# Performance work log

Measured on AMD Instinct MI355X. Metric: run time of the kernel, lower is better.

The kernel has to match this reference:

```python
import jax, jax.numpy as jnp
import numpy as np

PAD = 1  # deform_conv2d called with stride=1, padding=1, dilation=1 in forward


def _bilinear_gather(x, py, px):
    """Bilinear sample x [B,C,H,W] at float coords py,px [B,K,Ho,Wo].
    Out-of-bounds corners contribute zero (torchvision deform_conv2d semantics).
    Returns [B,C,K,Ho,Wo]."""
    B, C, H, W = x.shape
    y0 = jnp.floor(py)
    x0 = jnp.floor(px)
    y1, x1 = y0 + 1.0, x0 + 1.0
    wy1 = py - y0
    wy0 = 1.0 - wy1
    wx1 = px - x0
    wx0 = 1.0 - wx1
    x_flat = x.reshape(B, C, H * W)

    def corner(yi, xi, w):
        m = ((yi >= 0) & (yi < H) & (xi >= 0) & (xi < W)).astype(x.dtype)
        yc = jnp.clip(yi, 0, H - 1).astype(jnp.int32)
        xc = jnp.clip(xi, 0, W - 1).astype(jnp.int32)
        lin = (yc * W + xc).reshape(B, -1)  # [B, K*Ho*Wo]
        vals = jax.vmap(lambda xf, idx: jnp.take(xf, idx, axis=1))(x_flat, lin)
        vals = vals.reshape(B, C, *yi.shape[1:])  # [B,C,K,Ho,Wo]
        return vals * (w * m)[:, None]

    return (corner(y0, x0, wy0 * wx0) + corner(y0, x1, wy0 * wx1)
            + corner(y1, x0, wy1 * wx0) + corner(y1, x1, wy1 * wx1))


def reference(x, w_off, b_off, weight):
    B, C, H, W = x.shape
    O, Ci, kh, kw = weight.shape
    K = kh * kw
    # offset conv: Conv2d(C -> 2*k*k, kernel 3, stride 1, pad 1, groups=1)
    offset = jax.lax.conv_general_dilated(
        x, w_off, window_strides=(1, 1), padding=[(PAD, PAD), (PAD, PAD)],
        dimension_numbers=('NCHW', 'OIHW', 'NCHW')) + b_off[None, :, None, None]
    off = offset.reshape(B, K, 2, H, W)  # channel layout: (tap, [dy, dx])

    ky = jnp.repeat(jnp.arange(kh, dtype=x.dtype), kw)  # [K] kernel row index
    kx = jnp.tile(jnp.arange(kw, dtype=x.dtype), kh)    # [K] kernel col index
    ys = jnp.arange(H, dtype=x.dtype)[None, None, :, None]  # [1,1,H,1]
    xs = jnp.arange(W, dtype=x.dtype)[None, None, None, :]  # [1,1,1,W]
    py = ys + (ky - PAD)[None, :, None, None] + off[:, :, 0]  # [B,K,H,W]
    px = xs + (kx - PAD)[None, :, None, None] + off[:, :, 1]

    sampled = _bilinear_gather(x, py, px)  # [B,C,K,H,W]
    out = jnp.einsum('bckhw,ock->bohw', sampled, weight.reshape(O, Ci, K))
    return out


def setup_inputs() -> dict:
    key = jax.random.key(0)
    k1, k2, k3 = jax.random.split(key, 3)
    x = jax.random.normal(k1, (4, 64, 128, 128), dtype=jnp.float32)
    # small offset-conv weights -> modest learned offsets (realistic DCN behavior)
    w_off = jax.random.normal(k2, (18, 64, 3, 3), dtype=jnp.float32) * 0.01
    b_off = jnp.zeros((18,), dtype=jnp.float32)
    weight = jax.random.normal(k3, (64, 64, 3, 3), dtype=jnp.float32)
    return {'x': x, 'w_off': w_off, 'b_off': b_off, 'weight': weight}
```

## Files before the change

### kernel.cpp

```cpp
#include <hip/hip_runtime.h>
#include <math.h>

typedef _Float16 f16;
typedef _Float16 f16x8 __attribute__((ext_vector_type(8)));
typedef float f32x4 __attribute__((ext_vector_type(4)));

namespace {
constexpr int Bn = 4;
constexpr int Cn = 64;
constexpr int On = 64;
constexpr int Hn = 128;
constexpr int Wn = 128;
constexpr int Kn = 9;
constexpr int HWn = Hn * Wn;
constexpr int CKn = Cn * Kn;
constexpr int NPIX = Bn * HWn;
constexpr int SR = 72;
}

__global__ __launch_bounds__(256) void prep_weights(
    const float* __restrict__ w_off, const float* __restrict__ weight,
    f16* __restrict__ wofb, f16* __restrict__ wtb) {
  int t = blockIdx.x * 256 + threadIdx.x;
  if (t < Kn * On * Cn) {
    int c = t & 63, o = (t >> 6) & 63, k = t >> 12;
    wtb[t] = (f16)weight[((o << 6) + c) * 9 + k];
  }
  if (t < Kn * 32 * Cn) {
    int c = t & 63, o = (t >> 6) & 31, k = t >> 11;
    float v = (o < 18) ? w_off[((o << 6) + c) * 9 + k] : 0.f;
    wofb[t] = (f16)v;
  }
}

__global__ __launch_bounds__(256) void transpose_x(
    const float* __restrict__ x, f16* __restrict__ xt) {
  const int l = threadIdx.x & 63;
  const int cw = threadIdx.x >> 6;
  const int pixbase = blockIdx.x * 64;
  const int b = pixbase >> 14;
  const int hw = (pixbase & (HWn - 1)) + l;

  f16x8 v0, v1;
#pragma unroll
  for (int i = 0; i < 8; ++i) {
    v0[i] = (f16)x[((size_t)(b * Cn + cw * 16 + i)) * HWn + hw];
    v1[i] = (f16)x[((size_t)(b * Cn + cw * 16 + 8 + i)) * HWn + hw];
  }
  f16* dst = xt + ((size_t)(b * HWn + hw)) * 64 + cw * 16;
  *(f16x8*)dst = v0;
  *(f16x8*)(dst + 8) = v1;
}

__global__ __launch_bounds__(256) void offset_mfma(
    const f16* __restrict__ xt, const f16* __restrict__ wofb,
    const float* __restrict__ b_off, float* __restrict__ offset) {
  __shared__ __align__(16) f16 Sb[2][64 * SR];
  __shared__ __align__(16) f16 Wb[2][32 * SR];

  const int t = threadIdx.x;
  const int pixbase = blockIdx.x * 64;
  const int b = pixbase >> 14;
  const int y = (pixbase & (HWn - 1)) >> 7;
  const int xx0 = pixbase & (Wn - 1);
  const f16* xb = xt + ((size_t)b * HWn) * 64;

  const int px_s = t >> 2, cq = t & 3;
  const int lane = t & 63, wv = t >> 6;
  const int l15 = lane & 15, q = lane >> 4;
  const int m = wv & 1;
  const int nb = (wv >> 1) * 2;

  auto stage = [&](int k, int buf) {
    const int dy = k / 3 - 1, dx = k % 3 - 1;
    const int ys = y + dy, xs = xx0 + px_s + dx;
    f16* sdst = &Sb[buf][px_s * SR + cq * 16];
    if (ys >= 0 && ys < Hn && xs >= 0 && xs < Wn) {
      const f16* src = xb + (size_t)(ys * Wn + xs) * 64 + cq * 16;
      *(f16x8*)sdst = *(const f16x8*)src;
      *(f16x8*)(sdst + 8) = *(const f16x8*)(src + 8);
    } else {
      f16x8 z = {};
      *(f16x8*)sdst = z;
      *(f16x8*)(sdst + 8) = z;
    }
    const int o = t >> 3, part = t & 7;
    const f16* wsrc = wofb + (((size_t)(k * 32 + o)) << 6) + part * 8;
    *(f16x8*)&Wb[buf][o * SR + part * 8] = *(const f16x8*)wsrc;
  };

  f32x4 acc[2];
#pragma unroll
  for (int t2 = 0; t2 < 2; ++t2) acc[t2] = (f32x4){0.f, 0.f, 0.f, 0.f};

  stage(0, 0);
  __syncthreads();
  for (int k = 0; k < Kn; ++k) {
    const int cur = k & 1;
    if (k + 1 < Kn) stage(k + 1, 1 - cur);
#pragma unroll
    for (int s = 0; s < 2; ++s) {
      f16x8 af = *(const f16x8*)&Wb[cur][(m * 16 + l15) * SR + s * 32 + q * 8];
#pragma unroll
      for (int t2 = 0; t2 < 2; ++t2) {
        f16x8 bf = *(const f16x8*)
            &Sb[cur][((nb + t2) * 16 + l15) * SR + s * 32 + q * 8];
        acc[t2] = __builtin_amdgcn_mfma_f32_16x16x32_f16(af, bf, acc[t2],
                                                         0, 0, 0);
      }
    }
    __syncthreads();
  }

  float* ob = offset + ((size_t)b * HWn + y * Wn + xx0) * 18;
#pragma unroll
  for (int t2 = 0; t2 < 2; ++t2) {
#pragma unroll
    for (int r = 0; r < 4; ++r) {
      int o = m * 16 + q * 4 + r;
      if (o < 18) {
        int pxl = (nb + t2) * 16 + l15;
        ob[(size_t)pxl * 18 + o] = acc[t2][r] + b_off[o];
      }
    }
  }
}

__global__ __launch_bounds__(256, 4) void dcn_main(
    const f16* __restrict__ xt, const float* __restrict__ offset,
    const f16* __restrict__ wtb, float* __restrict__ out) {
  __shared__ __align__(16) f16 Sb[2][64 * SR];
  __shared__ __align__(16) f16 Wb[2][64 * SR];

  const int t = threadIdx.x;
  const int px_s = t >> 2, cq = t & 3;
  const int pxg = blockIdx.x * 64 + px_s;
  const int b = pxg >> 14;
  const int rem = pxg & (HWn - 1);
  const int y = rem >> 7;
  const int xx = rem & (Wn - 1);
  const f16* xb = xt + (((size_t)b) << 14) * 64;

  const int lane = t & 63, wv = t >> 6;
  const int l15 = lane & 15, q = lane >> 4;
  const int obase = wv * 16;

  float2 off9[9];
  {
    const float* ofp = offset + (size_t)pxg * 18;
#pragma unroll
    for (int k = 0; k < Kn; ++k) off9[k] = *(const float2*)(ofp + 2 * k);
  }

  auto stage = [&](int k, int buf) {
    const int dy = k / 3 - 1, dx = k % 3 - 1;
    float py = (float)(y + dy) + off9[k].x;
    float pxf = (float)(xx + dx) + off9[k].y;
    float y0f = floorf(py), x0f = floorf(pxf);
    int y0 = (int)y0f, x0 = (int)x0f;
    int y1 = y0 + 1, x1 = x0 + 1;
    float wy1 = py - y0f, wx1 = pxf - x0f;
    float wy0 = 1.f - wy1, wx0 = 1.f - wx1;
    float my0 = (y0 >= 0 && y0 < Hn) ? 1.f : 0.f;
    float my1 = (y1 >= 0 && y1 < Hn) ? 1.f : 0.f;
    float mx0 = (x0 >= 0 && x0 < Wn) ? 1.f : 0.f;
    float mx1 = (x1 >= 0 && x1 < Wn) ? 1.f : 0.f;
    float w00 = wy0 * wx0 * my0 * mx0;
    float w01 = wy0 * wx1 * my0 * mx1;
    float w10 = wy1 * wx0 * my1 * mx0;
    float w11 = wy1 * wx1 * my1 * mx1;
    int cy0 = min(max(y0, 0), Hn - 1), cy1 = min(max(y1, 0), Hn - 1);
    int cx0 = min(max(x0, 0), Wn - 1), cx1 = min(max(x1, 0), Wn - 1);
    const f16* r00 = xb + (size_t)(cy0 * Wn + cx0) * 64 + cq * 16;
    const f16* r01 = xb + (size_t)(cy0 * Wn + cx1) * 64 + cq * 16;
    const f16* r10 = xb + (size_t)(cy1 * Wn + cx0) * 64 + cq * 16;
    const f16* r11 = xb + (size_t)(cy1 * Wn + cx1) * 64 + cq * 16;
    f16* sdst = &Sb[buf][px_s * SR + cq * 16];
#pragma unroll
    for (int h = 0; h < 2; ++h) {
      f16x8 a = *(const f16x8*)(r00 + h * 8);
      f16x8 bb2 = *(const f16x8*)(r01 + h * 8);
      f16x8 c = *(const f16x8*)(r10 + h * 8);
      f16x8 d = *(const f16x8*)(r11 + h * 8);
      f16x8 v;
#pragma unroll
      for (int i = 0; i < 8; ++i) {
        float s = w00 * (float)a[i] + w01 * (float)bb2[i] +
                  w10 * (float)c[i] + w11 * (float)d[i];
        v[i] = (f16)s;
      }
      *(f16x8*)(sdst + h * 8) = v;
    }
    {
      const int o = t >> 2, part = t & 3;
      const f16* src = wtb + (((size_t)(k * 64 + o)) << 6) + part * 16;
      f16* dst = &Wb[buf][o * SR + part * 16];
      *(f16x8*)dst = *(const f16x8*)src;
      *(f16x8*)(dst + 8) = *(const f16x8*)(src + 8);
    }
  };

  f32x4 acc[4];
#pragma unroll
  for (int pt = 0; pt < 4; ++pt) acc[pt] = (f32x4){0.f, 0.f, 0.f, 0.f};

  stage(0, 0);
  __syncthreads();
  for (int k = 0; k < Kn; ++k) {
    const int cur = k & 1;
    if (k + 1 < Kn) stage(k + 1, 1 - cur);
#pragma unroll
    for (int s = 0; s < 2; ++s) {
      f16x8 af = *(const f16x8*)&Wb[cur][(obase + l15) * SR + s * 32 + q * 8];
#pragma unroll
      for (int pt = 0; pt < 4; ++pt) {
        f16x8 bf =
            *(const f16x8*)&Sb[cur][(pt * 16 + l15) * SR + s * 32 + q * 8];
        acc[pt] = __builtin_amdgcn_mfma_f32_16x16x32_f16(af, bf, acc[pt],
                                                         0, 0, 0);
      }
    }
    __syncthreads();
  }

  const int hw0 = (blockIdx.x * 64) & (HWn - 1);
  const int bb = (blockIdx.x * 64) >> 14;
  float* ob = out + (size_t)bb * On * HWn + hw0;
#pragma unroll
  for (int pt = 0; pt < 4; ++pt) {
#pragma unroll
    for (int r = 0; r < 4; ++r) {
      int o = obase + q * 4 + r;
      ob[(size_t)o * HWn + pt * 16 + l15] = acc[pt][r];
    }
  }
}

extern "C" void kernel_launch(void* const* d_in, const int* in_sizes, int n_in,
                              void* d_out, int out_size, void* d_ws, size_t ws_size,
                              hipStream_t stream) {
  const float* x = (const float*)d_in[0];
  const float* w_off = (const float*)d_in[1];
  const float* b_off = (const float*)d_in[2];
  const float* weight = (const float*)d_in[3];
  float* out = (float*)d_out;

  f16* xt = (f16*)d_ws;
  float* offset = (float*)(xt + (size_t)NPIX * Cn);
  f16* wtb = (f16*)(offset + (size_t)NPIX * 18);
  f16* wofb = wtb + Kn * On * Cn;

  prep_weights<<<dim3(144), dim3(256), 0, stream>>>(w_off, weight, wofb, wtb);
  transpose_x<<<dim3(NPIX / 64), dim3(256), 0, stream>>>(x, xt);
  offset_mfma<<<dim3(NPIX / 64), dim3(256), 0, stream>>>(xt, wofb, b_off,
                                                         offset);
  dcn_main<<<dim3(NPIX / 64), dim3(256), 0, stream>>>(xt, offset, wtb, out);
}
```

Measured before the change: 111.8 us.

## Batch three taps per sync, load weights into registers, use packed f16 bilinear

dcn_main now processes the nine kernel taps in three groups of three. Each group samples all three taps into three shared buffers, hits one barrier, then runs the MFMAs, instead of a per-tap double-buffered stage/compute loop. Weight fragments are read straight from global memory into registers, so the weight shared-memory buffer is gone. Bilinear interpolation is done as packed f16 vector math rather than per-element f32 FMAs. This cuts barriers and LDS traffic, but gives up overlap between gather and compute and loses some interpolation precision.

Measured after the change: 112.7 us. No clear change (+0.8%).

```diff
diff --git a/kernel.cpp b/kernel.cpp
--- a/kernel.cpp
+++ b/kernel.cpp
@@ -129,8 +129,7 @@
 __global__ __launch_bounds__(256, 4) void dcn_main(
     const f16* __restrict__ xt, const float* __restrict__ offset,
     const f16* __restrict__ wtb, float* __restrict__ out) {
-  __shared__ __align__(16) f16 Sb[2][64 * SR];
-  __shared__ __align__(16) f16 Wb[2][64 * SR];
+  __shared__ __align__(16) f16 Sb[3][64 * SR];
 
   const int t = threadIdx.x;
   const int px_s = t >> 2, cq = t & 3;
@@ -152,75 +151,70 @@
     for (int k = 0; k < Kn; ++k) off9[k] = *(const float2*)(ofp + 2 * k);
   }
 
-  auto stage = [&](int k, int buf) {
-    const int dy = k / 3 - 1, dx = k % 3 - 1;
-    float py = (float)(y + dy) + off9[k].x;
-    float pxf = (float)(xx + dx) + off9[k].y;
-    float y0f = floorf(py), x0f = floorf(pxf);
-    int y0 = (int)y0f, x0 = (int)x0f;
-    int y1 = y0 + 1, x1 = x0 + 1;
-    float wy1 = py - y0f, wx1 = pxf - x0f;
-    float wy0 = 1.f - wy1, wx0 = 1.f - wx1;
-    float my0 = (y0 >= 0 && y0 < Hn) ? 1.f : 0.f;
-    float my1 = (y1 >= 0 && y1 < Hn) ? 1.f : 0.f;
-    float mx0 = (x0 >= 0 && x0 < Wn) ? 1.f : 0.f;
-    float mx1 = (x1 >= 0 && x1 < Wn) ? 1.f : 0.f;
-    float w00 = wy0 * wx0 * my0 * mx0;
-    float w01 = wy0 * wx1 * my0 * mx1;
-    float w10 = wy1 * wx0 * my1 * mx0;
-    float w11 = wy1 * wx1 * my1 * mx1;
-    int cy0 = min(max(y0, 0), Hn - 1), cy1 = min(max(y1, 0), Hn - 1);
-    int cx0 = min(max(x0, 0), Wn - 1), cx1 = min(max(x1, 0), Wn - 1);
-    const f16* r00 = xb + (size_t)(cy0 * Wn + cx0) * 64 + cq * 16;
-    const f16* r01 = xb + (size_t)(cy0 * Wn + cx1) * 64 + cq * 16;
-    const f16* r10 = xb + (size_t)(cy1 * Wn + cx0) * 64 + cq * 16;
-    const f16* r11 = xb + (size_t)(cy1 * Wn + cx1) * 64 + cq * 16;
-    f16* sdst = &Sb[buf][px_s * SR + cq * 16];
-#pragma unroll
-    for (int h = 0; h < 2; ++h) {
-      f16x8 a = *(const f16x8*)(r00 + h * 8);
-      f16x8 bb2 = *(const f16x8*)(r01 + h * 8);
-      f16x8 c = *(const f16x8*)(r10 + h * 8);
-      f16x8 d = *(const f16x8*)(r11 + h * 8);
-      f16x8 v;
-#pragma unroll
-      for (int i = 0; i < 8; ++i) {
-        float s = w00 * (float)a[i] + w01 * (float)bb2[i] +
-                  w10 * (float)c[i] + w11 * (float)d[i];
-        v[i] = (f16)s;
+  f32x4 acc[4];
+#pragma unroll
+  for (int pt = 0; pt < 4; ++pt) acc[pt] = (f32x4){0.f, 0.f, 0.f, 0.f};
+
+  for (int g = 0; g < 3; ++g) {
+    if (g) __syncthreads();
+
+    f16x8 wf[3][2];
+#pragma unroll
+    for (int j = 0; j < 3; ++j)
+#pragma unroll
+      for (int s = 0; s < 2; ++s)
+        wf[j][s] = *(const f16x8*)(wtb +
+            (((size_t)((3 * g + j) * 64 + obase + l15)) << 6) + s * 32 + q * 8);
+
+#pragma unroll
+    for (int j = 0; j < 3; ++j) {
+      const int k = 3 * g + j;
+      const int dy = k / 3 - 1, dx = k % 3 - 1;
+      float py = (float)(y + dy) + off9[k].x;
+      float pxf = (float)(xx + dx) + off9[k].y;
+      float y0f = floorf(py), x0f = floorf(pxf);
+      int y0 = (int)y0f, x0 = (int)x0f;
+      int y1 = y0 + 1, x1 = x0 + 1;
+      float wy1 = py - y0f, wx1 = pxf - x0f;
+      float wy0 = 1.f - wy1, wx0 = 1.f - wx1;
+      float my0 = (y0 >= 0 && y0 < Hn) ? 1.f : 0.f;
+      float my1 = (y1 >= 0 && y1 < Hn) ? 1.f : 0.f;
+      float mx0 = (x0 >= 0 && x0 < Wn) ? 1.f : 0.f;
+      float mx1 = (x1 >= 0 && x1 < Wn) ? 1.f : 0.f;
+      f16 h00 = (f16)(wy0 * wx0 * my0 * mx0);
+      f16 h01 = (f16)(wy0 * wx1 * my0 * mx1);
+      f16 h10 = (f16)(wy1 * wx0 * my1 * mx0);
+      f16 h11 = (f16)(wy1 * wx1 * my1 * mx1);
+      int cy0 = min(max(y0, 0), Hn - 1), cy1 = min(max(y1, 0), Hn - 1);
+      int cx0 = min(max(x0, 0), Wn - 1), cx1 = min(max(x1, 0), Wn - 1);
+      const f16* r00 = xb + (size_t)(cy0 * Wn + cx0) * 64 + cq * 16;
+      const f16* r01 = xb + (size_t)(cy0 * Wn + cx1) * 64 + cq * 16;
+      const f16* r10 = xb + (size_t)(cy1 * Wn + cx0) * 64 + cq * 16;
+      const f16* r11 = xb + (size_t)(cy1 * Wn + cx1) * 64 + cq * 16;
+      f16* sdst = &Sb[j][px_s * SR + cq * 16];
+#pragma unroll
+      for (int h = 0; h < 2; ++h) {
+        f16x8 a = *(const f16x8*)(r00 + h * 8);
+        f16x8 b2 = *(const f16x8*)(r01 + h * 8);
+        f16x8 c = *(const f16x8*)(r10 + h * 8);
+        f16x8 d = *(const f16x8*)(r11 + h * 8);
+        f16x8 v = a * h00 + b2 * h01 + c * h10 + d * h11;
+        *(f16x8*)(sdst + h * 8) = v;
       }
-      *(f16x8*)(sdst + h * 8) = v;
-    }
-    {
-      const int o = t >> 2, part = t & 3;
-      const f16* src = wtb + (((size_t)(k * 64 + o)) << 6) + part * 16;
-      f16* dst = &Wb[buf][o * SR + part * 16];
-      *(f16x8*)dst = *(const f16x8*)src;
-      *(f16x8*)(dst + 8) = *(const f16x8*)(src + 8);
-    }
-  };
-
-  f32x4 acc[4];
-#pragma unroll
-  for (int pt = 0; pt < 4; ++pt) acc[pt] = (f32x4){0.f, 0.f, 0.f, 0.f};
-
-  stage(0, 0);
-  __syncthreads();
-  for (int k = 0; k < Kn; ++k) {
-    const int cur = k & 1;
-    if (k + 1 < Kn) stage(k + 1, 1 - cur);
-#pragma unroll
-    for (int s = 0; s < 2; ++s) {
-      f16x8 af = *(const f16x8*)&Wb[cur][(obase + l15) * SR + s * 32 + q * 8];
-#pragma unroll
-      for (int pt = 0; pt < 4; ++pt) {
-        f16x8 bf =
-            *(const f16x8*)&Sb[cur][(pt * 16 + l15) * SR + s * 32 + q * 8];
-        acc[pt] = __builtin_amdgcn_mfma_f32_16x16x32_f16(af, bf, acc[pt],
-                                                         0, 0, 0);
-      }
     }
     __syncthreads();
+
+#pragma unroll
+    for (int j = 0; j < 3; ++j)
+#pragma unroll
+      for (int s = 0; s < 2; ++s)
+#pragma unroll
+        for (int pt = 0; pt < 4; ++pt) {
+          f16x8 bf =
+              *(const f16x8*)&Sb[j][(pt * 16 + l15) * SR + s * 32 + q * 8];
+          acc[pt] = __builtin_amdgcn_mfma_f32_16x16x32_f16(wf[j][s], bf,
+                                                           acc[pt], 0, 0, 0);
+        }
   }
 
   const int hw0 = (blockIdx.x * 64) & (HWn - 1);
```
